# Optimization experiments

Hardware: AMD Instinct MI355X
Metric: run time of the kernel (lower is better)

The kernel has to match this reference:

```python
import jax, jax.numpy as jnp
import numpy as np

N_FEATURE = 12
SIGMA = 0.015
NODES = jnp.linspace(0.0, 0.3, 12)  # RBF centers, matches torch.linspace(0,0.3,12)

B, N, K, FIN = 16, 4096, 32, 4


def setup_inputs() -> dict:
    key = jax.random.key(0)
    ks = jax.random.split(key, 24)

    def make_d(ki, kd):
        idx = jax.random.randint(ki, (B, N, K), 0, N).astype(jnp.float32)
        dist = jax.random.uniform(kd, (B, N, K), minval=0.0, maxval=0.3)
        return jnp.stack([idx, dist], axis=-1)  # [B,N,K,2]

    def lin(kw, kb, fin, fout):
        W = jax.random.normal(kw, (fin, fout), jnp.float32) * (1.0 / np.sqrt(fin))
        b = jax.random.normal(kb, (fout,), jnp.float32) * 0.01
        return W, b

    x = jax.random.normal(ks[0], (B, N, FIN), jnp.float32)
    d1 = make_d(ks[1], ks[2])
    d0 = make_d(ks[3], ks[4])
    dm1 = make_d(ks[5], ks[6])
    mask = jnp.ones((B, N), dtype=bool)

    We, be = lin(ks[7], ks[8], FIN, N_FEATURE)
    Wm1, bm1 = lin(ks[9], ks[10], N_FEATURE + 12, N_FEATURE)
    Wu1, bu1 = lin(ks[11], ks[12], 2 * N_FEATURE, N_FEATURE)
    Wm0, bm0 = lin(ks[13], ks[14], N_FEATURE + 12, N_FEATURE)
    Wu0, bu0 = lin(ks[15], ks[16], 2 * N_FEATURE, N_FEATURE)
    Wmm1, bmm1 = lin(ks[17], ks[18], N_FEATURE + 12, N_FEATURE)
    Wum1, bum1 = lin(ks[19], ks[20], 2 * N_FEATURE, N_FEATURE)

    return {"x": x, "d1": d1, "d0": d0, "dm1": dm1, "mask": mask,
            "We": We, "be": be, "Wm1": Wm1, "bm1": bm1, "Wu1": Wu1, "bu1": bu1,
            "Wm0": Wm0, "bm0": bm0, "Wu0": Wu0, "bu0": bu0,
            "Wmm1": Wmm1, "bmm1": bmm1, "Wum1": Wum1, "bum1": bum1}


def _branch(h, d, Wm, bm, Wu, bu):
    # d: [B,N,K,2] -> channel 0 neighbor index, channel 1 distance
    idx = d[..., 0].astype(jnp.int32)                     # [B,N,K]
    rbf = jnp.exp(-((d[..., 1][..., None] - NODES) ** 2) / (2.0 * SIGMA ** 2))  # [B,N,K,12]
    hj = jax.vmap(lambda hb, ib: hb[ib])(h, idx)          # gather: [B,N,K,F]
    hd = jnp.concatenate([hj, rbf], axis=-1)              # [B,N,K,F+12]
    m = jax.nn.relu(hd @ Wm + bm).sum(axis=2)             # [B,N,F]
    return jax.nn.sigmoid(jnp.concatenate([h, m], axis=-1) @ Wu + bu)  # [B,N,F]


def reference(x, d1, d0, dm1, mask,
              We, be, Wm1, bm1, Wu1, bu1,
              Wm0, bm0, Wu0, bu0,
              Wmm1, bmm1, Wum1, bum1):
    h = jax.nn.relu(x @ We + be)                          # [B,N,12]
    h1 = _branch(h, d1, Wm1, bm1, Wu1, bu1)
    h0 = _branch(h, d0, Wm0, bm0, Wu0, bu0)
    hm1 = _branch(h, dm1, Wmm1, bmm1, Wum1, bum1)
    return (h1, h0, hm1)
```

## Files before the change

kernel.cpp:

```cpp
#include <hip/hip_runtime.h>
#include <hip/hip_fp16.h>
#include <math.h>

#define BBAT 16
#define NNODE 4096
#define KNB 32
#define NF 12
#define TBL 512
#define TMAIN 512
#define NPB 256

__device__ __forceinline__ __half2 u2h(unsigned int u) { __half2 h; __builtin_memcpy(&h, &u, 4); return h; }
__device__ __forceinline__ unsigned int h2u(__half2 h) { unsigned int u; __builtin_memcpy(&u, &h, 4); return u; }

__device__ __forceinline__ void phi_entry(int e, const float* __restrict__ Wm, float* ph)
{
    float dd = (float)e * (0.3f / (float)TBL);
    float rbf[12];
#pragma unroll
    for (int j = 0; j < 12; j++) {
        float t = dd - (0.3f / 11.0f) * (float)j;
        rbf[j] = expf(-2222.2222222222f * t * t);
    }
#pragma unroll
    for (int c = 0; c < NF; c++) {
        float s = 0.0f;
#pragma unroll
        for (int j = 0; j < 12; j++) s = fmaf(rbf[j], Wm[(12 + j) * NF + c], s);
        ph[c] = s;
    }
}

__device__ __forceinline__ void pack12(const float* v, uint4& a, uint2& bv)
{
    a.x  = h2u(__floats2half2_rn(v[0],  v[1]));
    a.y  = h2u(__floats2half2_rn(v[2],  v[3]));
    a.z  = h2u(__floats2half2_rn(v[4],  v[5]));
    a.w  = h2u(__floats2half2_rn(v[6],  v[7]));
    bv.x = h2u(__floats2half2_rn(v[8],  v[9]));
    bv.y = h2u(__floats2half2_rn(v[10], v[11]));
}

__global__ __launch_bounds__(256) void prep_kernel(
    const float* __restrict__ x, const float* __restrict__ We, const float* __restrict__ be,
    const float* __restrict__ Wm1, const float* __restrict__ bm1,
    const float* __restrict__ Wm0, const float* __restrict__ bm0,
    const float* __restrict__ Wmm1, const float* __restrict__ bmm1,
    uint4* __restrict__ gA, uint2* __restrict__ gB, uint4* __restrict__ tP)
{
    const int node = blockIdx.x * 256 + threadIdx.x;
    float4 xv = ((const float4*)x)[node];
    float hv[NF];
#pragma unroll
    for (int f = 0; f < NF; f++) {
        float s = be[f];
        s = fmaf(xv.x, We[0 * NF + f], s);
        s = fmaf(xv.y, We[1 * NF + f], s);
        s = fmaf(xv.z, We[2 * NF + f], s);
        s = fmaf(xv.w, We[3 * NF + f], s);
        hv[f] = fmaxf(s, 0.0f);
    }

#define DO_G(BR, WM, BM) {                                                     \
        float g[NF];                                                           \
        _Pragma("unroll") for (int c = 0; c < NF; c++) {                       \
            float s = BM[c];                                                   \
            _Pragma("unroll") for (int j = 0; j < NF; j++)                     \
                s = fmaf(hv[j], WM[j * NF + c], s);                            \
            g[c] = s;                                                          \
        }                                                                      \
        uint4 a; uint2 bv;                                                     \
        pack12(g, a, bv);                                                      \
        gA[(size_t)(BR) * 65536 + node] = a;                                   \
        gB[(size_t)(BR) * 65536 + node] = bv;                                  \
    }
    DO_G(0, Wm1, bm1)
    DO_G(1, Wm0, bm0)
    DO_G(2, Wmm1, bmm1)
#undef DO_G

    if (blockIdx.x < 3) {
        const int br = blockIdx.x;
        const float* Wm = (br == 0) ? Wm1 : (br == 1) ? Wm0 : Wmm1;
        for (int i = threadIdx.x; i < TBL; i += 256) {
            float p0[NF], p1[NF];
            phi_entry(i, Wm, p0);
            phi_entry(i + 1, Wm, p1);
            uint4 a0, a1; uint2 b0, b1;
            pack12(p0, a0, b0);
            pack12(p1, a1, b1);
            uint4 w0 = make_uint4(a0.x, a0.y, a0.z, a0.w);
            uint4 w1 = make_uint4(b0.x, b0.y, a1.x, a1.y);
            uint4 w2 = make_uint4(a1.z, a1.w, b1.x, b1.y);
            uint4* dst = tP + ((size_t)br * TBL + i) * 3;
            dst[0] = w0; dst[1] = w1; dst[2] = w2;
        }
    }
}

__global__ __launch_bounds__(TMAIN, 6) void main_kernel(
    const float* __restrict__ x, const float* __restrict__ We, const float* __restrict__ be,
    const uint4* __restrict__ gA, const uint2* __restrict__ gB, const uint4* __restrict__ tP,
    const float* __restrict__ d1, const float* __restrict__ d0, const float* __restrict__ dm1,
    const float* __restrict__ Wu1, const float* __restrict__ bu1,
    const float* __restrict__ Wu0, const float* __restrict__ bu0,
    const float* __restrict__ Wum1, const float* __restrict__ bum1,
    float* __restrict__ out)
{
    __shared__ uint4 tPl[TBL * 3];

    const int w = blockIdx.x;
    const int xcd = w & 7;
    const int k = w >> 3;
    const int slice = xcd + 8 * (k >> 4);
    const int chunk = k & 15;
    const int br = slice / BBAT;
    const int b  = slice % BBAT;

    const int tid = threadIdx.x;

    {
        const uint4* tPg = tP + (size_t)br * TBL * 3;
        for (int i = tid; i < TBL * 3; i += TMAIN) tPl[i] = tPg[i];
    }
    __syncthreads();

    const int nl = tid >> 1, half = tid & 1;
    const int n = chunk * NPB + nl;

    const float* dsel = (br == 0) ? d1 : (br == 1) ? d0 : dm1;
    const float* Wu   = (br == 0) ? Wu1 : (br == 1) ? Wu0 : Wum1;
    const float* bu   = (br == 0) ? bu1 : (br == 1) ? bu0 : bum1;

    const uint4* gAg = gA + (size_t)slice * NNODE;
    const uint2* gBg = gB + (size_t)slice * NNODE;

    float m[NF];
#pragma unroll
    for (int f = 0; f < NF; f++) m[f] = 0.0f;

    const float4* dp = (const float4*)(dsel + ((size_t)b * NNODE + n) * (size_t)(KNB * 2)) + half * 8;

#define ACC(O, G, T0, T1) {                                                    \
        __half2 t0 = u2h(T0), t1 = u2h(T1);                                    \
        __half2 phi = __hfma2(f2, __hsub2(t1, t0), t0);                        \
        __half2 s2 = __hadd2(u2h(G), phi);                                     \
        float2 sf = __half22float2(s2);                                        \
        m[O]     += fmaxf(sf.x, 0.0f);                                         \
        m[O + 1] += fmaxf(sf.y, 0.0f);                                         \
    }

#pragma unroll
    for (int kt = 0; kt < 2; kt++) {
        float4 e0 = dp[kt * 4 + 0];
        float4 e1 = dp[kt * 4 + 1];
        float4 e2 = dp[kt * 4 + 2];
        float4 e3 = dp[kt * 4 + 3];
        float idxf[8] = { e0.x, e0.z, e1.x, e1.z, e2.x, e2.z, e3.x, e3.z };
        float dist[8] = { e0.y, e0.w, e1.y, e1.w, e2.y, e2.w, e3.y, e3.w };
#pragma unroll
        for (int ee = 0; ee < 8; ee++) {
            int j = (int)idxf[ee];
            uint4 ga = gAg[j];
            uint2 gb = gBg[j];
            float uu = dist[ee] * ((float)TBL / 0.3f);
            int i = (int)uu;
            i = min(i, TBL - 1);
            float fr = uu - (float)i;
            __half2 f2 = __float2half2_rn(fr);
            const uint4* tp = &tPl[i * 3];
            uint4 r0 = tp[0];
            uint4 r1 = tp[1];
            uint4 r2 = tp[2];
            ACC(0,  ga.x, r0.x, r1.z)
            ACC(2,  ga.y, r0.y, r1.w)
            ACC(4,  ga.z, r0.z, r2.x)
            ACC(6,  ga.w, r0.w, r2.y)
            ACC(8,  gb.x, r1.x, r2.z)
            ACC(10, gb.y, r1.y, r2.w)
        }
    }
#undef ACC

#pragma unroll
    for (int f = 0; f < NF; f++) m[f] += __shfl_xor(m[f], 1);

    float4 xv = ((const float4*)x)[(size_t)b * NNODE + n];
    float hv[NF];
#pragma unroll
    for (int f = 0; f < NF; f++) {
        float s = be[f];
        s = fmaf(xv.x, We[0 * NF + f], s);
        s = fmaf(xv.y, We[1 * NF + f], s);
        s = fmaf(xv.z, We[2 * NF + f], s);
        s = fmaf(xv.w, We[3 * NF + f], s);
        hv[f] = fmaxf(s, 0.0f);
    }

    const int f0 = half * 6;
    float ov[6];
#pragma unroll
    for (int ff = 0; ff < 6; ff++) {
        const int f = f0 + ff;
        float a = bu[f];
#pragma unroll
        for (int j = 0; j < NF; j++) a = fmaf(hv[j], Wu[j * NF + f], a);
#pragma unroll
        for (int j = 0; j < NF; j++) a = fmaf(m[j], Wu[(NF + j) * NF + f], a);
        ov[ff] = 1.0f / (1.0f + __expf(-a));
    }
    float* op = out + ((size_t)slice * NNODE + n) * NF + f0;
    ((float2*)op)[0] = make_float2(ov[0], ov[1]);
    ((float2*)op)[1] = make_float2(ov[2], ov[3]);
    ((float2*)op)[2] = make_float2(ov[4], ov[5]);
}

extern "C" void kernel_launch(void* const* d_in, const int* in_sizes, int n_in,
                              void* d_out, int out_size, void* d_ws, size_t ws_size,
                              hipStream_t stream)
{
    const float* x    = (const float*)d_in[0];
    const float* d1   = (const float*)d_in[1];
    const float* d0   = (const float*)d_in[2];
    const float* dm1  = (const float*)d_in[3];
    const float* We   = (const float*)d_in[5];
    const float* be   = (const float*)d_in[6];
    const float* Wm1  = (const float*)d_in[7];
    const float* bm1  = (const float*)d_in[8];
    const float* Wu1  = (const float*)d_in[9];
    const float* bu1  = (const float*)d_in[10];
    const float* Wm0  = (const float*)d_in[11];
    const float* bm0  = (const float*)d_in[12];
    const float* Wu0  = (const float*)d_in[13];
    const float* bu0  = (const float*)d_in[14];
    const float* Wmm1 = (const float*)d_in[15];
    const float* bmm1 = (const float*)d_in[16];
    const float* Wum1 = (const float*)d_in[17];
    const float* bum1 = (const float*)d_in[18];

    char* ws = (char*)d_ws;
    uint4* gA = (uint4*)ws;
    uint2* gB = (uint2*)(ws + 3145728);
    uint4* tP = (uint4*)(ws + 4718592);

    prep_kernel<<<dim3(256), 256, 0, stream>>>(
        x, We, be, Wm1, bm1, Wm0, bm0, Wmm1, bmm1, gA, gB, tP);
    main_kernel<<<dim3(768), TMAIN, 0, stream>>>(
        x, We, be, gA, gB, tP, d1, d0, dm1,
        Wu1, bu1, Wu0, bu0, Wum1, bum1, (float*)d_out);
}
```

Baseline: 180.2 us.

## Interleave gathered neighbor features into 32B records and software-pipeline gathers

The two separate gather arrays (16B + 8B per node) are merged into one padded 32-byte record, so each neighbor gather touches one contiguous segment instead of two distant ones. The main kernel now loads all edge data into registers before the table copy and barrier, and it double-buffers the neighbor gathers in groups of four so loads overlap with the interpolation math. Launch bounds drop from 6 to 4 waves per SIMD to leave room for the extra registers, at the cost of lower occupancy and a larger workspace footprint.

```diff
diff --git a/kernel.cpp b/kernel.cpp
--- a/kernel.cpp
+++ b/kernel.cpp
@@ -46,7 +46,7 @@
     const float* __restrict__ Wm1, const float* __restrict__ bm1,
     const float* __restrict__ Wm0, const float* __restrict__ bm0,
     const float* __restrict__ Wmm1, const float* __restrict__ bmm1,
-    uint4* __restrict__ gA, uint2* __restrict__ gB, uint4* __restrict__ tP)
+    uint4* __restrict__ gP, uint4* __restrict__ tP)
 {
     const int node = blockIdx.x * 256 + threadIdx.x;
     float4 xv = ((const float4*)x)[node];
@@ -71,8 +71,9 @@
         }                                                                      \
         uint4 a; uint2 bv;                                                     \
         pack12(g, a, bv);                                                      \
-        gA[(size_t)(BR) * 65536 + node] = a;                                   \
-        gB[(size_t)(BR) * 65536 + node] = bv;                                  \
+        uint4* dst = gP + ((size_t)(BR) * 65536 + node) * 2;                   \
+        dst[0] = a;                                                            \
+        dst[1] = make_uint4(bv.x, bv.y, 0u, 0u);                               \
     }
     DO_G(0, Wm1, bm1)
     DO_G(1, Wm0, bm0)
@@ -98,9 +99,9 @@
     }
 }
 
-__global__ __launch_bounds__(TMAIN, 6) void main_kernel(
+__global__ __launch_bounds__(TMAIN, 4) void main_kernel(
     const float* __restrict__ x, const float* __restrict__ We, const float* __restrict__ be,
-    const uint4* __restrict__ gA, const uint2* __restrict__ gB, const uint4* __restrict__ tP,
+    const uint4* __restrict__ gP, const uint4* __restrict__ tP,
     const float* __restrict__ d1, const float* __restrict__ d0, const float* __restrict__ dm1,
     const float* __restrict__ Wu1, const float* __restrict__ bu1,
     const float* __restrict__ Wu0, const float* __restrict__ bu0,
@@ -118,6 +119,15 @@
     const int b  = slice % BBAT;
 
     const int tid = threadIdx.x;
+    const int nl = tid >> 1, half = tid & 1;
+    const int n = chunk * NPB + nl;
+
+    const float* dsel = (br == 0) ? d1 : (br == 1) ? d0 : dm1;
+
+    const float4* dp = (const float4*)(dsel + ((size_t)b * NNODE + n) * (size_t)(KNB * 2)) + half * 8;
+    float4 dreg[8];
+#pragma unroll
+    for (int r = 0; r < 8; r++) dreg[r] = dp[r];
 
     {
         const uint4* tPg = tP + (size_t)br * TBL * 3;
@@ -125,21 +135,24 @@
     }
     __syncthreads();
 
-    const int nl = tid >> 1, half = tid & 1;
-    const int n = chunk * NPB + nl;
-
-    const float* dsel = (br == 0) ? d1 : (br == 1) ? d0 : dm1;
-    const float* Wu   = (br == 0) ? Wu1 : (br == 1) ? Wu0 : Wum1;
-    const float* bu   = (br == 0) ? bu1 : (br == 1) ? bu0 : bum1;
-
-    const uint4* gAg = gA + (size_t)slice * NNODE;
-    const uint2* gBg = gB + (size_t)slice * NNODE;
+    const float* Wu = (br == 0) ? Wu1 : (br == 1) ? Wu0 : Wum1;
+    const float* bu = (br == 0) ? bu1 : (br == 1) ? bu0 : bum1;
+
+    const uint4* gPg = gP + (size_t)slice * NNODE * 2;
+
+    int   jv[16];
+    float uv[16];
+#pragma unroll
+    for (int r = 0; r < 8; r++) {
+        jv[2 * r]     = (int)dreg[r].x;
+        jv[2 * r + 1] = (int)dreg[r].z;
+        uv[2 * r]     = dreg[r].y * ((float)TBL / 0.3f);
+        uv[2 * r + 1] = dreg[r].w * ((float)TBL / 0.3f);
+    }
 
     float m[NF];
 #pragma unroll
     for (int f = 0; f < NF; f++) m[f] = 0.0f;
-
-    const float4* dp = (const float4*)(dsel + ((size_t)b * NNODE + n) * (size_t)(KNB * 2)) + half * 8;
 
 #define ACC(O, G, T0, T1) {                                                    \
         __half2 t0 = u2h(T0), t1 = u2h(T1);                                    \
@@ -150,36 +163,46 @@
         m[O + 1] += fmaxf(sf.y, 0.0f);                                         \
     }
 
-#pragma unroll
-    for (int kt = 0; kt < 2; kt++) {
-        float4 e0 = dp[kt * 4 + 0];
-        float4 e1 = dp[kt * 4 + 1];
-        float4 e2 = dp[kt * 4 + 2];
-        float4 e3 = dp[kt * 4 + 3];
-        float idxf[8] = { e0.x, e0.z, e1.x, e1.z, e2.x, e2.z, e3.x, e3.z };
-        float dist[8] = { e0.y, e0.w, e1.y, e1.w, e2.y, e2.w, e3.y, e3.w };
-#pragma unroll
-        for (int ee = 0; ee < 8; ee++) {
-            int j = (int)idxf[ee];
-            uint4 ga = gAg[j];
-            uint2 gb = gBg[j];
-            float uu = dist[ee] * ((float)TBL / 0.3f);
-            int i = (int)uu;
-            i = min(i, TBL - 1);
-            float fr = uu - (float)i;
-            __half2 f2 = __float2half2_rn(fr);
-            const uint4* tp = &tPl[i * 3];
-            uint4 r0 = tp[0];
-            uint4 r1 = tp[1];
-            uint4 r2 = tp[2];
-            ACC(0,  ga.x, r0.x, r1.z)
-            ACC(2,  ga.y, r0.y, r1.w)
-            ACC(4,  ga.z, r0.z, r2.x)
-            ACC(6,  ga.w, r0.w, r2.y)
-            ACC(8,  gb.x, r1.x, r2.z)
-            ACC(10, gb.y, r1.y, r2.w)
-        }
-    }
+#define ISSUE(GA, GB, BASE)                                                    \
+    _Pragma("unroll") for (int e = 0; e < 4; e++) {                            \
+        const uint4* p = gPg + 2 * jv[(BASE) + e];                             \
+        GA[e] = p[0];                                                          \
+        GB[e] = *(const uint2*)(p + 1);                                        \
+    }
+
+#define PROCESS(GA, GB, BASE)                                                  \
+    _Pragma("unroll") for (int e = 0; e < 4; e++) {                            \
+        float uu = uv[(BASE) + e];                                             \
+        int i = (int)uu;                                                       \
+        i = min(i, TBL - 1);                                                   \
+        float fr = uu - (float)i;                                              \
+        __half2 f2 = __float2half2_rn(fr);                                     \
+        const uint4* tp = &tPl[i * 3];                                         \
+        uint4 r0 = tp[0];                                                      \
+        uint4 r1 = tp[1];                                                      \
+        uint4 r2 = tp[2];                                                      \
+        uint4 ga = GA[e]; uint2 gb = GB[e];                                    \
+        ACC(0,  ga.x, r0.x, r1.z)                                              \
+        ACC(2,  ga.y, r0.y, r1.w)                                              \
+        ACC(4,  ga.z, r0.z, r2.x)                                              \
+        ACC(6,  ga.w, r0.w, r2.y)                                              \
+        ACC(8,  gb.x, r1.x, r2.z)                                              \
+        ACC(10, gb.y, r1.y, r2.w)                                              \
+    }
+
+    uint4 gaA[4], gaB[4];
+    uint2 gbA[4], gbB[4];
+    ISSUE(gaA, gbA, 0)
+    ISSUE(gaB, gbB, 4)
+    PROCESS(gaA, gbA, 0)
+    ISSUE(gaA, gbA, 8)
+    PROCESS(gaB, gbB, 4)
+    ISSUE(gaB, gbB, 12)
+    PROCESS(gaA, gbA, 8)
+    PROCESS(gaB, gbB, 12)
+
+#undef PROCESS
+#undef ISSUE
 #undef ACC
 
 #pragma unroll
@@ -239,13 +262,12 @@
     const float* bum1 = (const float*)d_in[18];
 
     char* ws = (char*)d_ws;
-    uint4* gA = (uint4*)ws;
-    uint2* gB = (uint2*)(ws + 3145728);
-    uint4* tP = (uint4*)(ws + 4718592);
+    uint4* gP = (uint4*)ws;
+    uint4* tP = (uint4*)(ws + 6291456);
 
     prep_kernel<<<dim3(256), 256, 0, stream>>>(
-        x, We, be, Wm1, bm1, Wm0, bm0, Wmm1, bmm1, gA, gB, tP);
+        x, We, be, Wm1, bm1, Wm0, bm0, Wmm1, bmm1, gP, tP);
     main_kernel<<<dim3(768), TMAIN, 0, stream>>>(
-        x, We, be, gA, gB, tP, d1, d0, dm1,
+        x, We, be, gP, tP, d1, d0, dm1,
         Wu1, bu1, Wu0, bu0, Wum1, bum1, (float*)d_out);
 }
```

Measured after the change: 197.4 us. 1.1x slower.
